# Kernel tuning notes

Hardware: AMD Instinct MI355X
Metric: run time of the kernel (lower is better)

The kernel has to match this reference:

```python
import jax, jax.numpy as jnp
import numpy as np

B, V, C, D = 32, 64, 32, 256
VOCAB = 20000
NUM_T = 1000


def _run_lstm(x, Wih, Whh, b):
    # x: [T, B, H_in]; torch-style single-layer LSTM with zero initial state
    T, Bb, _ = x.shape
    H = Whh.shape[1]
    def step(carry, xt):
        h, c = carry
        z = xt @ Wih.T + h @ Whh.T + b
        i, f, g, o = jnp.split(z, 4, axis=-1)
        c = jax.nn.sigmoid(f) * c + jax.nn.sigmoid(i) * jnp.tanh(g)
        h = jax.nn.sigmoid(o) * jnp.tanh(c)
        return (h, c), h
    h0 = jnp.zeros((Bb, H), x.dtype)
    _, ys = jax.lax.scan(step, (h0, h0), x)
    return ys


def _forward(input_seqs, masks, lengths, seq_time_step, code_masks, emb, WQ1, WK1,
             decay, initial, lstm_Wih, lstm_Whh, lstm_b, hs_Wih, hs_Whh, hs_b,
             whk_W, whk_b, w1_W, w1_b, w2_W, w2_b, fuse_W, fuse_b, lab_W, lab_b,
             betas, Wdiff, diffusion_time_t, normal_noise):
    Bb, Vv, Cc = input_seqs.shape
    tok = input_seqs.reshape(-1, Cc)                      # [B*V, C]
    x = emb[tok]                                          # [B*V, C, D]
    q = x @ WQ1.T
    k = x @ WK1.T
    dp = jnp.einsum('bcd,bed->bce', q, k)                 # [B*V, C, C]
    cm = code_masks.reshape(-1, Cc)
    dp = dp - cm[:, None, :] - cm[:, :, None]
    sp = jax.nn.softmax(dp / jnp.sqrt(jnp.float32(D)), axis=-1)
    femb = jnp.einsum('bce,bed->bcd', sp, x)              # attended code embeddings
    femb = ((cm - 1e20) / -1e20)[:, :, None] * femb       # zero out padded codes
    dec = decay[tok][..., None]                           # [B*V, C, 1]
    ini = initial[tok][..., None]
    t = seq_time_step.reshape(-1)[:, None, None]          # [B*V, 1, 1]
    gate = jax.nn.sigmoid(dec * t + ini)                  # time-decay gate
    vv = jnp.einsum('bcx,bcd->bd', gate, femb)            # [B*V, D] visit vector
    vv = vv.reshape(Bb, Vv, -1).transpose(1, 0, 2)        # [V, B, D]

    lstm_out = _run_lstm(vv, lstm_Wih, lstm_Whh, lstm_b)  # [V, B, D]
    t_lstm = lstm_out.transpose(1, 0, 2)                  # [B, V, D]
    hiddenstate = _run_lstm(lstm_out, hs_Wih, hs_Whh, hs_b).transpose(1, 0, 2)

    # Vectorized form of the original per-step python loop.
    # NOTE: the original always uses e_k = t_lstm_out[:, 0:1, :] (step 0) -- kept faithfully.
    e_k = t_lstm[:, 0:1, :]                               # [B, 1, D]
    whp = hiddenstate[:, :-1, :] @ whk_W.T + whk_b        # [B, V-1, D]
    cat = jnp.concatenate([jnp.broadcast_to(e_k, whp.shape), whp], axis=-1)
    attn = jax.nn.softmax(jnp.tanh(cat @ w1_W.T + w1_b) @ w2_W.T + w2_b, axis=-1)
    rest = e_k * attn[..., 0:1] + whp * attn[..., 1:2]
    aligned = jnp.concatenate([e_k, rest], axis=1)        # [B, V, D]

    alpha = jnp.cumprod(1.0 - betas)[diffusion_time_t][:, None, None]
    noisy = aligned * jnp.sqrt(alpha) + normal_noise * jnp.sqrt(1.0 - alpha)
    predicted_noise = noisy @ Wdiff                       # surrogate for UNetModel (source not provided)
    gen = aligned + (normal_noise - predicted_noise)

    fused = jnp.concatenate([t_lstm, gen], axis=-1) @ fuse_W.T + fuse_b   # [B, V, D]
    mask_final = (jnp.arange(Vv)[None, :] == (lengths - 1)[:, None]).astype(fused.dtype)
    final = (fused * mask_final[:, :, None]).sum(axis=1)  # select last valid visit
    return final @ lab_W.T + lab_b                        # [B, 2]


def setup_inputs() -> dict:
    key = jax.random.key(0)
    ks = jax.random.split(key, 20)
    s = 0.05
    n = lambda i, shp: jax.random.normal(ks[i], shp, jnp.float32) * s
    emb = jax.random.normal(ks[0], (VOCAB + 1, D), jnp.float32) * 0.02
    emb = emb.at[VOCAB].set(0.0)  # padding_idx row
    return {
        'input_seqs': jax.random.randint(ks[1], (B, V, C), 0, VOCAB),
        'masks': jnp.zeros((B, V), jnp.float32),
        'lengths': jax.random.randint(ks[2], (B,), 1, V + 1),
        'seq_time_step': jax.random.uniform(ks[3], (B, V), jnp.float32),
        'code_masks': jnp.zeros((B, V, C), jnp.float32),
        'emb': emb,
        'WQ1': n(4, (D, D)), 'WK1': n(5, (D, D)),
        'decay': jnp.full((VOCAB + 1,), -0.1, jnp.float32),
        'initial': jnp.full((VOCAB + 1,), 1.0, jnp.float32),
        'lstm_Wih': n(6, (4 * D, D)), 'lstm_Whh': n(7, (4 * D, D)),
        'lstm_b': jnp.zeros((4 * D,), jnp.float32),
        'hs_Wih': n(8, (4 * D, D)), 'hs_Whh': n(9, (4 * D, D)),
        'hs_b': jnp.zeros((4 * D,), jnp.float32),
        'whk_W': n(10, (D, D)), 'whk_b': jnp.zeros((D,), jnp.float32),
        'w1_W': n(11, (64, 2 * D)), 'w1_b': jnp.zeros((64,), jnp.float32),
        'w2_W': n(12, (2, 64)), 'w2_b': jnp.zeros((2,), jnp.float32),
        'fuse_W': n(13, (D, 2 * D)), 'fuse_b': jnp.zeros((D,), jnp.float32),
        'lab_W': n(14, (2, D)), 'lab_b': jnp.zeros((2,), jnp.float32),
        'betas': jnp.linspace(1e-4, 0.02, NUM_T, dtype=jnp.float32),
        'Wdiff': n(15, (D, D)),
        'diffusion_time_t': jax.random.randint(ks[16], (B,), 0, NUM_T),
        'normal_noise': jax.random.normal(ks[17], (B, V, D), jnp.float32),
    }


def reference(input_seqs, masks, lengths, seq_time_step, code_masks, emb, WQ1, WK1,
              decay, initial, lstm_Wih, lstm_Whh, lstm_b, hs_Wih, hs_Whh, hs_b,
              whk_W, whk_b, w1_W, w1_b, w2_W, w2_b, fuse_W, fuse_b, lab_W, lab_b,
              betas, Wdiff, diffusion_time_t, normal_noise):
    return _forward(input_seqs, masks, lengths, seq_time_step, code_masks, emb, WQ1, WK1,
                    decay, initial, lstm_Wih, lstm_Whh, lstm_b, hs_Wih, hs_Whh, hs_b,
                    whk_W, whk_b, w1_W, w1_b, w2_W, w2_b, fuse_W, fuse_b, lab_W, lab_b,
                    betas, Wdiff, diffusion_time_t, normal_noise)
```

## Files before the change

kernel.cpp:

```cpp
#include <hip/hip_runtime.h>
#include <hip/hip_bf16.h>
#include <cmath>

typedef __attribute__((ext_vector_type(8))) short bf16x8;
typedef __attribute__((ext_vector_type(4))) float f32x4;
typedef __attribute__((ext_vector_type(4))) int i32x4;
typedef __attribute__((ext_vector_type(2))) unsigned int u32x2;

__device__ __forceinline__ float bf2f(unsigned short u) {
    unsigned int x = ((unsigned int)u) << 16;
    return __builtin_bit_cast(float, x);
}
__device__ __forceinline__ unsigned short f2bf(float f) {
    unsigned int x = __builtin_bit_cast(unsigned int, f);
    unsigned int lsb = (x >> 16) & 1u;
    x += 0x7fffu + lsb;
    return (unsigned short)(x >> 16);
}
__device__ __forceinline__ float sigm(float z) {
    return 1.f / (1.f + __expf(-z));
}
__device__ __forceinline__ float rcpf(float x) { return __builtin_amdgcn_rcpf(x); }
__device__ __forceinline__ float sigm_f(float z) { return rcpf(1.f + __expf(-z)); }
__device__ __forceinline__ float tanh_f(float z) { return 1.f - 2.f * rcpf(1.f + __expf(2.f * z)); }

__device__ __forceinline__ long ldg_sc8l(const void* p) {
    long r;
    asm volatile("global_load_dwordx2 %0, %1, off sc1" : "=v"(r) : "v"(p) : "memory");
    return r;
}
__device__ __forceinline__ u32x2 ldg_sc_u2(const void* p) {
    u32x2 r;
    asm volatile("global_load_dwordx2 %0, %1, off sc1" : "=v"(r) : "v"(p) : "memory");
    return r;
}
__device__ __forceinline__ void stg_sc_u2(void* p, u32x2 v) {
    asm volatile("global_store_dwordx2 %0, %1, off sc1" :: "v"(p), "v"(v) : "memory");
}
__device__ __forceinline__ void stg_sc_b(void* p, int v) {
    asm volatile("global_store_byte %0, %1, off sc1" :: "v"(p), "v"(v) : "memory");
}

__global__ void __launch_bounds__(256) pack_all(
    const float* __restrict__ Whh1, const float* __restrict__ Wih2,
    const float* __restrict__ Whh2, const float* __restrict__ Wih1,
    const float* __restrict__ WQ1, const float* __restrict__ WK1,
    const float* __restrict__ betas, const int* __restrict__ dift,
    const float* __restrict__ whk_W, const float* __restrict__ fuse_W,
    const float* __restrict__ w1_W,
    long* __restrict__ Wq, float* __restrict__ cs,
    unsigned short* __restrict__ W1h, unsigned short* __restrict__ M_pk,
    float* __restrict__ alpha, int* __restrict__ flags,
    float* __restrict__ whkT, float* __restrict__ fuseT,
    float* __restrict__ w1T) {
    int blk = blockIdx.x, tid = threadIdx.x;
    if (blk < 384) {
        int R = blk * 8 + (tid >> 5);
        int mat = R >> 10;
        int n = R & 1023;
        int t32 = tid & 31;
        const float* src = (mat == 0) ? Whh1 : (mat == 1 ? Wih2 : Whh2);
        const float* rp = src + (size_t)n * 256 + t32 * 8;
        float v[8];
        float mx = 0.f;
        for (int j = 0; j < 8; ++j) { v[j] = rp[j]; mx = fmaxf(mx, fabsf(v[j])); }
        for (int m = 1; m <= 16; m <<= 1) mx = fmaxf(mx, __shfl_xor(mx, m));
        float inv = mx > 0.f ? 127.f / mx : 0.f;
        unsigned int lo = 0, hi = 0;
        for (int j = 0; j < 4; ++j) {
            int iv = __float2int_rn(v[j] * inv);
            lo |= ((unsigned int)(unsigned char)(signed char)iv) << (8 * j);
            int iv2 = __float2int_rn(v[4 + j] * inv);
            hi |= ((unsigned int)(unsigned char)(signed char)iv2) << (8 * j);
        }
        int g = n >> 8, rem = n & 255;
        int w8 = rem >> 5, dt = (rem >> 4) & 1, cc = rem & 15;
        int t8 = g * 2 + dt;
        int kb = t32 >> 2, q = t32 & 3;
        unsigned int* dst = (unsigned int*)Wq +
            ((size_t)((mat * 512 + w8 * 64 + t8 * 8 + kb) * 64) + q * 16 + cc) * 2;
        dst[0] = lo;
        dst[1] = hi;
        if (t32 == 0) cs[mat * 1024 + n] = mx / 16129.f;
    } else if (blk < 512) {
        int cch = (blk - 384) * 256 + tid;
        int nt = cch >> 9;
        int r = cch & 511;
        int kb = r >> 6;
        int lane = r & 63;
        int grow = nt * 16 + (lane & 15);
        int k0 = kb * 32 + (lane >> 4) * 8;
        const float* sp = Wih1 + (size_t)grow * 256 + k0;
        bf16x8 hi;
        for (int j = 0; j < 8; ++j) hi[j] = (short)f2bf(sp[j]);
        *reinterpret_cast<bf16x8*>(W1h + (size_t)cch * 8) = hi;
    } else if (blk == 512) {
        if (tid < 32) {
            int tb = dift[tid];
            float p = 1.f;
            for (int i = 0; i <= tb; ++i) p *= (1.f - betas[i]);
            alpha[tid] = p;
        }
    } else if (blk == 513) {
        for (int i = tid; i < 4096; i += 256) flags[i] = 0;
    } else if (blk < 578) {
        int gid = (blk - 514) * 256 + tid;
        for (int i = 0; i < 4; ++i) {
            int e = gid + i * 16384;
            int k = e >> 8, dd = e & 255;
            whkT[e] = whk_W[(size_t)dd * 256 + k];
        }
    } else if (blk < 706) {
        int gid = (blk - 578) * 256 + tid;
        for (int i = 0; i < 4; ++i) {
            int e = gid + i * 32768;
            int k = e >> 8, dd = e & 255;
            fuseT[e] = fuse_W[(size_t)dd * 512 + k];
        }
    } else if (blk < 738) {
        int gid = (blk - 706) * 256 + tid;
        for (int i = 0; i < 4; ++i) {
            int e = gid + i * 8192;
            int k = e >> 6, j = e & 63;
            w1T[e] = w1_W[(size_t)j * 512 + k];
        }
    } else {
        __shared__ unsigned short As[256][32];
        __shared__ unsigned short Bs[256][32];
        int bx = blk - 738;
        int e0 = (bx >> 3) << 5;
        int f0 = (bx & 7) << 5;
        int col = tid & 31, rr = tid >> 5;
        for (int rep = 0; rep < 32; ++rep) {
            int d = rep * 8 + rr;
            As[d][col] = f2bf(WQ1[d * 256 + e0 + col]);
            Bs[d][col] = f2bf(WK1[d * 256 + f0 + col]);
        }
        __syncthreads();
        int el = tid & 31;
        int fl0 = tid >> 5;
        for (int i = 0; i < 4; ++i) {
            int fl = fl0 + 8 * i;
            float acc = 0.f;
            for (int d = 0; d < 256; ++d)
                acc += bf2f(As[d][el]) * bf2f(Bs[d][fl]);
            int e = e0 + el, f = f0 + fl;
            int kb = e >> 5, r = (e >> 3) & 3, j = e & 7;
            int nb = f >> 4;
            int lane = (r << 4) | (f & 15);
            M_pk[(((nb * 8 + kb) * 64) + lane) * 8 + j] = f2bf(acc);
        }
    }
}

__global__ void __launch_bounds__(256) eprep(const float* __restrict__ emb,
                                             const unsigned short* __restrict__ M_pk,
                                             unsigned short* __restrict__ Ep) {
    __shared__ __align__(16) unsigned short x_bf[32 * 256];
    int v0 = blockIdx.x * 32;
    int tid = threadIdx.x;
    for (int it = 0; it < 8; ++it) {
        int fidx = it * 256 + tid;
        int cc = fidx >> 6;
        int f4 = fidx & 63;
        int row = v0 + cc;
        float4 vx = make_float4(0.f, 0.f, 0.f, 0.f);
        if (row < 20001)
            vx = *(reinterpret_cast<const float4*>(emb + (size_t)row * 256) + f4);
        int colx = f4 * 4;
        ushort4 w;
        w.x = f2bf(vx.x); w.y = f2bf(vx.y); w.z = f2bf(vx.z); w.w = f2bf(vx.w);
        *reinterpret_cast<ushort4*>(&x_bf[cc * 256 + (colx ^ ((cc & 7) << 3))]) = w;
    }
    __syncthreads();
    int wv = tid >> 6, lane = tid & 63, lr = lane & 15, lk = lane >> 4;
    f32x4 acc[2][4];
    for (int a = 0; a < 2; ++a)
        for (int n = 0; n < 4; ++n) acc[a][n] = (f32x4){0.f, 0.f, 0.f, 0.f};
    for (int kb = 0; kb < 8; ++kb) {
        bf16x8 afr[2];
        for (int mb = 0; mb < 2; ++mb) {
            int row = mb * 16 + lr;
            int colx = kb * 32 + lk * 8;
            afr[mb] = *reinterpret_cast<const bf16x8*>(&x_bf[row * 256 + (colx ^ ((row & 7) << 3))]);
        }
        for (int nbi = 0; nbi < 4; ++nbi) {
            int nb = wv * 4 + nbi;
            bf16x8 bfr = *reinterpret_cast<const bf16x8*>(M_pk + (((nb * 8 + kb) * 64) + lane) * 8);
            acc[0][nbi] = __builtin_amdgcn_mfma_f32_16x16x32_bf16(afr[0], bfr, acc[0][nbi], 0, 0, 0);
            acc[1][nbi] = __builtin_amdgcn_mfma_f32_16x16x32_bf16(afr[1], bfr, acc[1][nbi], 0, 0, 0);
        }
    }
    for (int mb = 0; mb < 2; ++mb)
        for (int nbi = 0; nbi < 4; ++nbi)
            for (int r = 0; r < 4; ++r) {
                int row = mb * 16 + lk * 4 + r;
                int col = wv * 64 + nbi * 16 + lr;
                if (v0 + row < 20001)
                    Ep[(size_t)(v0 + row) * 256 + col] = f2bf(acc[mb][nbi][r]);
            }
}

__global__ void __launch_bounds__(256) attn_bags(
    const int* __restrict__ seqs, const float* __restrict__ tstep,
    const float* __restrict__ cmask, const float* __restrict__ emb,
    const float* __restrict__ decay, const float* __restrict__ initial,
    const unsigned short* __restrict__ Ep, float* __restrict__ vv) {
    __shared__ __align__(16) unsigned short x_bf[32 * 256];
    __shared__ __align__(16) unsigned short t1_bf[32 * 256];
    __shared__ float dp_f[32 * 33];
    __shared__ float gate_sh[32];
    __shared__ float cm_sh[32];
    __shared__ int tok_sh[32];
    __shared__ float w_sh[32];

    int bag = blockIdx.x;
    int tid = threadIdx.x;

    if (tid < 32) {
        int tok = seqs[bag * 32 + tid];
        tok_sh[tid] = tok;
        float cm = cmask[bag * 32 + tid];
        cm_sh[tid] = cm;
        float tt = tstep[bag];
        float g = sigm(decay[tok] * tt + initial[tok]);
        g *= (cm - 1e20f) / (-1e20f);
        gate_sh[tid] = g;
    }
    __syncthreads();

    for (int it = 0; it < 8; ++it) {
        int fidx = it * 256 + tid;
        int c = fidx >> 6;
        int f4 = fidx & 63;
        const float4* src = reinterpret_cast<const float4*>(emb + (size_t)tok_sh[c] * 256) + f4;
        float4 vx = *src;
        int colx = f4 * 4;
        int eidx = c * 256 + (colx ^ ((c & 7) << 3));
        ushort4 w;
        w.x = f2bf(vx.x); w.y = f2bf(vx.y); w.z = f2bf(vx.z); w.w = f2bf(vx.w);
        *reinterpret_cast<ushort4*>(&x_bf[eidx]) = w;
    }
    for (int it = 0; it < 4; ++it) {
        int idx = it * 256 + tid;
        int cc = idx >> 5;
        int colx = (idx & 31) * 8;
        bf16x8 e = *reinterpret_cast<const bf16x8*>(Ep + (size_t)tok_sh[cc] * 256 + colx);
        *reinterpret_cast<bf16x8*>(&t1_bf[cc * 256 + (colx ^ ((cc & 7) << 3))]) = e;
    }
    __syncthreads();

    int wv = tid >> 6;
    int lane = tid & 63;
    int lr = lane & 15;
    int lk = lane >> 4;

    {
        int mb = wv >> 1, nb2 = wv & 1;
        f32x4 dacc = (f32x4){0.f, 0.f, 0.f, 0.f};
        for (int kb = 0; kb < 8; ++kb) {
            int cola = kb * 32 + lk * 8;
            int rowa = mb * 16 + lr;
            bf16x8 afr = *reinterpret_cast<const bf16x8*>(&t1_bf[rowa * 256 + (cola ^ ((rowa & 7) << 3))]);
            int rowb = nb2 * 16 + lr;
            bf16x8 bfr = *reinterpret_cast<const bf16x8*>(&x_bf[rowb * 256 + (cola ^ ((rowb & 7) << 3))]);
            dacc = __builtin_amdgcn_mfma_f32_16x16x32_bf16(afr, bfr, dacc, 0, 0, 0);
        }
        for (int r = 0; r < 4; ++r) {
            int c = mb * 16 + lk * 4 + r;
            int e = nb2 * 16 + lr;
            dp_f[c * 33 + e] = dacc[r];
        }
    }
    __syncthreads();

    if (tid < 32) {
        int c = tid;
        float cmc = cm_sh[c];
        float lg[32];
        float mx = -1e30f;
        for (int e = 0; e < 32; ++e) {
            float l = (dp_f[c * 33 + e] - cmc - cm_sh[e]) * 0.0625f;
            lg[e] = l;
            mx = fmaxf(mx, l);
        }
        float s = 0.f;
        for (int e = 0; e < 32; ++e) { float ex = __expf(lg[e] - mx); lg[e] = ex; s += ex; }
        float inv = 1.f / s;
        for (int e = 0; e < 32; ++e) dp_f[c * 33 + e] = lg[e] * inv;
    }
    __syncthreads();
    if (tid < 32) {
        int e = tid;
        float a2 = 0.f;
        for (int c = 0; c < 32; ++c) a2 += gate_sh[c] * dp_f[c * 33 + e];
        w_sh[e] = a2;
    }
    __syncthreads();

    float accv = 0.f;
    int d = tid;
    for (int e = 0; e < 32; ++e)
        accv += w_sh[e] * bf2f(x_bf[e * 256 + (d ^ ((e & 7) << 3))]);
    vv[(size_t)bag * 256 + d] = accv;
}

__global__ void __launch_bounds__(256) x1_mfma(const float* __restrict__ vv,
                                               const unsigned short* __restrict__ W1h,
                                               const float* __restrict__ lstm_b,
                                               unsigned short* __restrict__ X1bf) {
    __shared__ __align__(16) unsigned short xs[32 * 256];
    int blk = blockIdx.x;
    int rb = blk >> 3, gb = blk & 7;
    int tid = threadIdx.x;
    for (int it = 0; it < 8; ++it) {
        int idx = it * 256 + tid;
        int row = idx >> 6, f4 = idx & 63;
        float4 v = *reinterpret_cast<const float4*>(vv + (size_t)(rb * 32 + row) * 256 + f4 * 4);
        ushort4 w;
        w.x = f2bf(v.x); w.y = f2bf(v.y); w.z = f2bf(v.z); w.w = f2bf(v.w);
        *reinterpret_cast<ushort4*>(&xs[row * 256 + ((f4 * 4) ^ ((row & 7) << 3))]) = w;
    }
    __syncthreads();
    int wv = tid >> 6, lane = tid & 63, cl = lane & 15, kh = lane >> 4;
    f32x4 acc[2][2];
    for (int n = 0; n < 2; ++n) {
        int nt = gb * 8 + wv * 2 + n;
        float bz = lstm_b[nt * 16 + cl];
        acc[n][0] = (f32x4){bz, bz, bz, bz};
        acc[n][1] = (f32x4){bz, bz, bz, bz};
    }
    #pragma unroll
    for (int kb = 0; kb < 8; ++kb) {
        int k = kb * 32 + kh * 8;
        bf16x8 a0 = *reinterpret_cast<const bf16x8*>(&xs[cl * 256 + (k ^ ((cl & 7) << 3))]);
        bf16x8 a1 = *reinterpret_cast<const bf16x8*>(&xs[(16 + cl) * 256 + (k ^ (((16 + cl) & 7) << 3))]);
        for (int n = 0; n < 2; ++n) {
            int nt = gb * 8 + wv * 2 + n;
            size_t o = ((size_t)(nt * 8 + kb) * 64 + lane) * 8;
            bf16x8 bh = *reinterpret_cast<const bf16x8*>(W1h + o);
            acc[n][0] = __builtin_amdgcn_mfma_f32_16x16x32_bf16(a0, bh, acc[n][0], 0, 0, 0);
            acc[n][1] = __builtin_amdgcn_mfma_f32_16x16x32_bf16(a1, bh, acc[n][1], 0, 0, 0);
        }
    }
    for (int n = 0; n < 2; ++n) {
        int nt = gb * 8 + wv * 2 + n;
        int g = nt * 16 + cl;
        int dX = g & 255, gt = g >> 8;
        for (int mt = 0; mt < 2; ++mt)
            for (int r = 0; r < 4; ++r) {
                int row = rb * 32 + mt * 16 + kh * 4 + r;
                int b = row >> 6, t = row & 63;
                X1bf[((size_t)t * 32 + b) * 1024 + dX * 4 + gt] = f2bf(acc[n][mt][r]);
            }
    }
}

__global__ void __launch_bounds__(512, 1) lstm_persist(
    const long* __restrict__ Wq, const float* __restrict__ cs,
    const unsigned short* __restrict__ X1bf, const float* __restrict__ hs_b,
    const int* __restrict__ lengths,
    unsigned short* __restrict__ h1bf, unsigned short* __restrict__ h2bf,
    signed char* h1q, unsigned short* p1, int* flags) {
    int role = blockIdx.x;
    int half = role & 1;
    int kind = role >> 1;
    int tid = threadIdx.x;
    int w = tid >> 6, lane = tid & 63, c = lane & 15, q = lane >> 4;

    long wt[64];
    #pragma unroll
    for (int t8 = 0; t8 < 8; ++t8)
        #pragma unroll
        for (int kb = 0; kb < 8; ++kb)
            wt[t8 * 8 + kb] = Wq[(size_t)((kind * 512 + w * 64 + t8 * 8 + kb) * 64) + lane];
    float csv[8];
    #pragma unroll
    for (int t8 = 0; t8 < 8; ++t8) {
        int g = t8 >> 1, dt = t8 & 1;
        csv[t8] = cs[kind * 1024 + g * 256 + w * 32 + dt * 16 + c];
    }

    if (kind == 0) {
        __shared__ signed char hq[2][16][272];
        float cstate[8] = {0.f, 0.f, 0.f, 0.f, 0.f, 0.f, 0.f, 0.f};
        int B0 = half * 16 + q * 4;
        int dbase = w * 32;
        int vstar[4];
        #pragma unroll
        for (int r = 0; r < 4; ++r) vstar[r] = lengths[B0 + r] - 1;
        for (int t = 0; t < 64; ++t) {
            ushort4 xv[8];
            #pragma unroll
            for (int dt = 0; dt < 2; ++dt)
                #pragma unroll
                for (int r = 0; r < 4; ++r) {
                    int B = B0 + r, d = dbase + dt * 16 + c;
                    xv[dt * 4 + r] = *reinterpret_cast<const ushort4*>(
                        X1bf + ((size_t)(t * 32 + B) * 1024 + d * 4));
                }
            i32x4 acc[8];
            #pragma unroll
            for (int i = 0; i < 8; ++i) acc[i] = (i32x4){0, 0, 0, 0};
            if (t > 0) {
                int pb = (t - 1) & 1;
                long a[8];
                #pragma unroll
                for (int kb = 0; kb < 8; ++kb)
                    a[kb] = *reinterpret_cast<const long*>(&hq[pb][c][kb * 32 + q * 8]);
                #pragma unroll
                for (int t8 = 0; t8 < 8; ++t8)
                    #pragma unroll
                    for (int kb = 0; kb < 8; ++kb)
                        acc[t8] = __builtin_amdgcn_mfma_i32_16x16x32_i8(
                            a[kb], wt[t8 * 8 + kb], acc[t8], 0, 0, 0);
            }
            #pragma unroll
            for (int dt = 0; dt < 2; ++dt)
                #pragma unroll
                for (int r = 0; r < 4; ++r) {
                    int idx = dt * 4 + r;
                    ushort4 x = xv[idx];
                    float zi = (float)acc[0 + dt][r] * csv[0 + dt] + bf2f(x.x);
                    float zf = (float)acc[2 + dt][r] * csv[2 + dt] + bf2f(x.y);
                    float zg = (float)acc[4 + dt][r] * csv[4 + dt] + bf2f(x.z);
                    float zo = (float)acc[6 + dt][r] * csv[6 + dt] + bf2f(x.w);
                    float cn = sigm_f(zf) * cstate[idx] + sigm_f(zi) * tanh_f(zg);
                    float hn = sigm_f(zo) * tanh_f(cn);
                    cstate[idx] = cn;
                    int B = B0 + r, d = dbase + dt * 16 + c;
                    if (t == 0 || t == vstar[r])
                        h1bf[(size_t)(t * 32 + B) * 256 + d] = f2bf(hn);
                    int hv = __float2int_rn(hn * 127.f);
                    hq[t & 1][q * 4 + r][d] = (signed char)hv;
                    stg_sc_b(h1q + (size_t)(t * 32 + B) * 256 + d, hv);
                }
            asm volatile("s_waitcnt vmcnt(0)" ::: "memory");
            if (lane == 0)
                __hip_atomic_store(flags + t * 16 + half * 8 + w, 1,
                                   __ATOMIC_RELAXED, __HIP_MEMORY_SCOPE_AGENT);
            __syncthreads();
        }
    } else if (kind == 1) {
        long acur[8], anext[8];
        {
            const int* f = flags + half * 8;
            while (1) {
                int v = 1;
                if (lane < 8)
                    v = __hip_atomic_load(f + lane, __ATOMIC_RELAXED, __HIP_MEMORY_SCOPE_AGENT);
                if (__all(v != 0)) break;
                __builtin_amdgcn_s_sleep(1);
            }
            __builtin_amdgcn_sched_barrier(0);
            const signed char* hb = h1q + (size_t)(half * 16) * 256;
            #pragma unroll
            for (int kb = 0; kb < 8; ++kb)
                acur[kb] = ldg_sc8l(hb + c * 256 + kb * 32 + q * 8);
            asm volatile("s_waitcnt vmcnt(0)" ::: "memory");
            __builtin_amdgcn_sched_barrier(0);
        }
        for (int s = 0; s < 64; ++s) {
            if (s < 63) {
                const int* f = flags + (s + 1) * 16 + half * 8;
                while (1) {
                    int v = 1;
                    if (lane < 8)
                        v = __hip_atomic_load(f + lane, __ATOMIC_RELAXED, __HIP_MEMORY_SCOPE_AGENT);
                    if (__all(v != 0)) break;
                    __builtin_amdgcn_s_sleep(1);
                }
                __builtin_amdgcn_sched_barrier(0);
                const signed char* hb = h1q + (size_t)((s + 1) * 32 + half * 16) * 256;
                #pragma unroll
                for (int kb = 0; kb < 8; ++kb)
                    anext[kb] = ldg_sc8l(hb + c * 256 + kb * 32 + q * 8);
            }
            i32x4 acc[8];
            #pragma unroll
            for (int i = 0; i < 8; ++i) acc[i] = (i32x4){0, 0, 0, 0};
            #pragma unroll
            for (int t8 = 0; t8 < 8; ++t8)
                #pragma unroll
                for (int kb = 0; kb < 8; ++kb)
                    acc[t8] = __builtin_amdgcn_mfma_i32_16x16x32_i8(
                        acur[kb], wt[t8 * 8 + kb], acc[t8], 0, 0, 0);
            #pragma unroll
            for (int t8 = 0; t8 < 8; ++t8) {
                int g = t8 >> 1, dt = t8 & 1;
                int n = g * 256 + w * 32 + dt * 16 + c;
                u32x2 pv;
                pv.x = (unsigned int)f2bf((float)acc[t8][0] * csv[t8]) |
                       ((unsigned int)f2bf((float)acc[t8][1] * csv[t8]) << 16);
                pv.y = (unsigned int)f2bf((float)acc[t8][2] * csv[t8]) |
                       ((unsigned int)f2bf((float)acc[t8][3] * csv[t8]) << 16);
                stg_sc_u2(p1 + ((size_t)(s * 2 + half) * 1024 + n) * 16 + q * 4, pv);
            }
            asm volatile("s_waitcnt vmcnt(0)" ::: "memory");
            __builtin_amdgcn_sched_barrier(0);
            if (lane == 0)
                __hip_atomic_store(flags + 1024 + s * 16 + half * 8 + w, 1,
                                   __ATOMIC_RELAXED, __HIP_MEMORY_SCOPE_AGENT);
            #pragma unroll
            for (int kb = 0; kb < 8; ++kb) acur[kb] = anext[kb];
        }
    } else {
        __shared__ signed char hq2[2][16][272];
        float cstate[8] = {0.f, 0.f, 0.f, 0.f, 0.f, 0.f, 0.f, 0.f};
        float bias[8];
        #pragma unroll
        for (int t8 = 0; t8 < 8; ++t8) {
            int g = t8 >> 1, dt = t8 & 1;
            bias[t8] = hs_b[g * 256 + w * 32 + dt * 16 + c];
        }
        int B0 = half * 16 + q * 4;
        int dbase = w * 32;
        int vstar[4];
        #pragma unroll
        for (int r = 0; r < 4; ++r) vstar[r] = lengths[B0 + r] - 1;
        u32x2 pvc[8], pvn[8];
        {
            const int* fp = flags + 1024 + half * 8 + w;
            while (__hip_atomic_load(fp, __ATOMIC_RELAXED, __HIP_MEMORY_SCOPE_AGENT) == 0)
                __builtin_amdgcn_s_sleep(1);
            __builtin_amdgcn_sched_barrier(0);
            #pragma unroll
            for (int t8 = 0; t8 < 8; ++t8) {
                int g = t8 >> 1, dt = t8 & 1;
                int n = g * 256 + w * 32 + dt * 16 + c;
                pvc[t8] = ldg_sc_u2(p1 + ((size_t)half * 1024 + n) * 16 + q * 4);
            }
        }
        for (int s = 0; s < 64; ++s) {
            if (s < 63) {
                const int* fp = flags + 1024 + (s + 1) * 16 + half * 8 + w;
                while (__hip_atomic_load(fp, __ATOMIC_RELAXED, __HIP_MEMORY_SCOPE_AGENT) == 0)
                    __builtin_amdgcn_s_sleep(1);
                __builtin_amdgcn_sched_barrier(0);
                #pragma unroll
                for (int t8 = 0; t8 < 8; ++t8) {
                    int g = t8 >> 1, dt = t8 & 1;
                    int n = g * 256 + w * 32 + dt * 16 + c;
                    pvn[t8] = ldg_sc_u2(p1 + ((size_t)((s + 1) * 2 + half) * 1024 + n) * 16 + q * 4);
                }
                asm volatile("s_waitcnt vmcnt(8)" ::: "memory");
            } else {
                asm volatile("s_waitcnt vmcnt(0)" ::: "memory");
            }
            __builtin_amdgcn_sched_barrier(0);
            i32x4 acc[8];
            #pragma unroll
            for (int i = 0; i < 8; ++i) acc[i] = (i32x4){0, 0, 0, 0};
            if (s > 0) {
                int pb = (s - 1) & 1;
                long a[8];
                #pragma unroll
                for (int kb = 0; kb < 8; ++kb)
                    a[kb] = *reinterpret_cast<const long*>(&hq2[pb][c][kb * 32 + q * 8]);
                #pragma unroll
                for (int t8 = 0; t8 < 8; ++t8)
                    #pragma unroll
                    for (int kb = 0; kb < 8; ++kb)
                        acc[t8] = __builtin_amdgcn_mfma_i32_16x16x32_i8(
                            a[kb], wt[t8 * 8 + kb], acc[t8], 0, 0, 0);
            }
            #pragma unroll
            for (int dt = 0; dt < 2; ++dt)
                #pragma unroll
                for (int r = 0; r < 4; ++r) {
                    int idx = dt * 4 + r;
                    float p_i = bf2f((unsigned short)((r < 2 ? pvc[0 + dt].x : pvc[0 + dt].y) >> ((r & 1) * 16)));
                    float p_f = bf2f((unsigned short)((r < 2 ? pvc[2 + dt].x : pvc[2 + dt].y) >> ((r & 1) * 16)));
                    float p_g = bf2f((unsigned short)((r < 2 ? pvc[4 + dt].x : pvc[4 + dt].y) >> ((r & 1) * 16)));
                    float p_o = bf2f((unsigned short)((r < 2 ? pvc[6 + dt].x : pvc[6 + dt].y) >> ((r & 1) * 16)));
                    float zi = (float)acc[0 + dt][r] * csv[0 + dt] + p_i + bias[0 + dt];
                    float zf = (float)acc[2 + dt][r] * csv[2 + dt] + p_f + bias[2 + dt];
                    float zg = (float)acc[4 + dt][r] * csv[4 + dt] + p_g + bias[4 + dt];
                    float zo = (float)acc[6 + dt][r] * csv[6 + dt] + p_o + bias[6 + dt];
                    float cn = sigm_f(zf) * cstate[idx] + sigm_f(zi) * tanh_f(zg);
                    float hn = sigm_f(zo) * tanh_f(cn);
                    cstate[idx] = cn;
                    int B = B0 + r, d = dbase + dt * 16 + c;
                    if (s == vstar[r] - 1)
                        h2bf[(size_t)(s * 32 + B) * 256 + d] = f2bf(hn);
                    hq2[s & 1][q * 4 + r][d] = (signed char)__float2int_rn(hn * 127.f);
                }
            __syncthreads();
            #pragma unroll
            for (int t8 = 0; t8 < 8; ++t8) pvc[t8] = pvn[t8];
        }
    }
}

__global__ void __launch_bounds__(256) tail_k(
    const int* __restrict__ lengths,
    const unsigned short* __restrict__ h1, const unsigned short* __restrict__ h2,
    const float* __restrict__ whkT, const float* __restrict__ whk_b,
    const float* __restrict__ w1T, const float* __restrict__ w1_b,
    const float* __restrict__ w2_W, const float* __restrict__ w2_b,
    const float* __restrict__ fuseT, const float* __restrict__ fuse_b,
    const float* __restrict__ lab_W, const float* __restrict__ lab_b,
    const float* __restrict__ Wdiff, const float* __restrict__ alpha,
    const float* __restrict__ noise, float* __restrict__ out) {
    __shared__ float ek[256], tv[256], hs[256], whp[256], a1s[64];
    __shared__ float noisy_s[256], fin[512], fused_s[256], attn_s[2];
    int b = blockIdx.x, tid = threadIdx.x;
    int vstar = lengths[b] - 1;
    {
        ek[tid] = bf2f(h1[(size_t)b * 256 + tid]);
        tv[tid] = bf2f(h1[((size_t)vstar * 32 + b) * 256 + tid]);
        if (vstar > 0)
            hs[tid] = bf2f(h2[((size_t)(vstar - 1) * 32 + b) * 256 + tid]);
    }
    __syncthreads();

    float aligned;
    if (vstar > 0) {
        float s0 = 0.f, s1 = 0.f, s2 = 0.f, s3 = 0.f;
        for (int k = 0; k < 256; k += 4) {
            s0 += whkT[(k + 0) * 256 + tid] * hs[k + 0];
            s1 += whkT[(k + 1) * 256 + tid] * hs[k + 1];
            s2 += whkT[(k + 2) * 256 + tid] * hs[k + 2];
            s3 += whkT[(k + 3) * 256 + tid] * hs[k + 3];
        }
        whp[tid] = whk_b[tid] + s0 + s1 + s2 + s3;
        __syncthreads();
        if (tid < 64) {
            float a0 = 0.f, a1 = 0.f, a2 = 0.f, a3 = 0.f;
            for (int k = 0; k < 256; k += 4) {
                a0 += w1T[(k + 0) * 64 + tid] * ek[k + 0];
                a1 += w1T[(k + 1) * 64 + tid] * ek[k + 1];
                a2 += w1T[(k + 2) * 64 + tid] * ek[k + 2];
                a3 += w1T[(k + 3) * 64 + tid] * ek[k + 3];
            }
            for (int k = 0; k < 256; k += 4) {
                a0 += w1T[(256 + k + 0) * 64 + tid] * whp[k + 0];
                a1 += w1T[(256 + k + 1) * 64 + tid] * whp[k + 1];
                a2 += w1T[(256 + k + 2) * 64 + tid] * whp[k + 2];
                a3 += w1T[(256 + k + 3) * 64 + tid] * whp[k + 3];
            }
            a1s[tid] = tanhf(w1_b[tid] + a0 + a1 + a2 + a3);
        }
        __syncthreads();
        if (tid < 2) {
            float a3 = w2_b[tid];
            const float* wr2 = w2_W + tid * 64;
            for (int k = 0; k < 64; ++k) a3 += wr2[k] * a1s[k];
            attn_s[tid] = a3;
        }
        __syncthreads();
        float m = fmaxf(attn_s[0], attn_s[1]);
        float e0 = __expf(attn_s[0] - m), e1 = __expf(attn_s[1] - m);
        float inv = 1.f / (e0 + e1);
        aligned = ek[tid] * (e0 * inv) + whp[tid] * (e1 * inv);
    } else {
        aligned = ek[tid];
    }

    float al = alpha[b];
    float sa = sqrtf(al), sb = sqrtf(1.f - al);
    float nz = noise[((size_t)b * 64 + vstar) * 256 + tid];
    noisy_s[tid] = aligned * sa + nz * sb;
    __syncthreads();
    {
        float p0 = 0.f, p1v = 0.f, p2 = 0.f, p3 = 0.f;
        for (int k = 0; k < 256; k += 4) {
            p0 += noisy_s[k + 0] * Wdiff[(size_t)(k + 0) * 256 + tid];
            p1v += noisy_s[k + 1] * Wdiff[(size_t)(k + 1) * 256 + tid];
            p2 += noisy_s[k + 2] * Wdiff[(size_t)(k + 2) * 256 + tid];
            p3 += noisy_s[k + 3] * Wdiff[(size_t)(k + 3) * 256 + tid];
        }
        float gen = aligned + nz - (p0 + p1v + p2 + p3);
        fin[tid] = tv[tid];
        fin[256 + tid] = gen;
    }
    __syncthreads();
    {
        float f0 = 0.f, f1 = 0.f, f2 = 0.f, f3 = 0.f;
        for (int k = 0; k < 512; k += 4) {
            f0 += fuseT[(k + 0) * 256 + tid] * fin[k + 0];
            f1 += fuseT[(k + 1) * 256 + tid] * fin[k + 1];
            f2 += fuseT[(k + 2) * 256 + tid] * fin[k + 2];
            f3 += fuseT[(k + 3) * 256 + tid] * fin[k + 3];
        }
        fused_s[tid] = fuse_b[tid] + f0 + f1 + f2 + f3;
    }
    __syncthreads();
    if (tid < 2) {
        float o = lab_b[tid];
        const float* lw = lab_W + tid * 256;
        for (int k = 0; k < 256; ++k) o += lw[k] * fused_s[k];
        out[b * 2 + tid] = o;
    }
}

extern "C" void kernel_launch(void* const* d_in, const int* in_sizes, int n_in,
                              void* d_out, int out_size, void* d_ws, size_t ws_size,
                              hipStream_t stream) {
    const int*   seqs    = (const int*)  d_in[0];
    const int*   lengths = (const int*)  d_in[2];
    const float* tstep   = (const float*)d_in[3];
    const float* cmask   = (const float*)d_in[4];
    const float* emb     = (const float*)d_in[5];
    const float* WQ1     = (const float*)d_in[6];
    const float* WK1     = (const float*)d_in[7];
    const float* decay   = (const float*)d_in[8];
    const float* initial = (const float*)d_in[9];
    const float* Wih1    = (const float*)d_in[10];
    const float* Whh1    = (const float*)d_in[11];
    const float* lstm_b  = (const float*)d_in[12];
    const float* Wih2    = (const float*)d_in[13];
    const float* Whh2    = (const float*)d_in[14];
    const float* hs_b    = (const float*)d_in[15];
    const float* whk_W   = (const float*)d_in[16];
    const float* whk_b   = (const float*)d_in[17];
    const float* w1_W    = (const float*)d_in[18];
    const float* w1_b    = (const float*)d_in[19];
    const float* w2_W    = (const float*)d_in[20];
    const float* w2_b    = (const float*)d_in[21];
    const float* fuse_W  = (const float*)d_in[22];
    const float* fuse_b  = (const float*)d_in[23];
    const float* lab_W   = (const float*)d_in[24];
    const float* lab_b   = (const float*)d_in[25];
    const float* betas   = (const float*)d_in[26];
    const float* Wdiff   = (const float*)d_in[27];
    const int*   dift    = (const int*)  d_in[28];
    const float* noise   = (const float*)d_in[29];
    float* out = (float*)d_out;

    float* ws = (float*)d_ws;
    size_t off = 0;
    auto alloc = [&](size_t nfloats) { size_t r = off; off += (nfloats + 63) & ~(size_t)63; return r; };
    unsigned short* M_pk  = (unsigned short*)(ws + alloc(32768));
    float*          alpha = ws + alloc(64);
    float*          cs    = ws + alloc(3072);
    int*            flags = (int*)(ws + alloc(4096));
    float*          vv    = ws + alloc(524288);
    unsigned short* X1bf  = (unsigned short*)(ws + alloc(1048576));
    unsigned short* h1bf  = (unsigned short*)(ws + alloc(262144));
    unsigned short* h2bf  = (unsigned short*)(ws + alloc(262144));
    unsigned short* p1    = (unsigned short*)(ws + alloc(1048576));
    long*           Wq    = (long*)(ws + alloc(196608));
    unsigned short* W1h   = (unsigned short*)(ws + alloc(131072));
    float*          whkT  = ws + alloc(65536);
    float*          fuseT = ws + alloc(131072);
    float*          w1T   = ws + alloc(32768);
    signed char*    h1q   = (signed char*)(ws + alloc(131072));
    unsigned short* Ep    = (unsigned short*)(ws + alloc(2560128));

    pack_all<<<802, 256, 0, stream>>>(Whh1, Wih2, Whh2, Wih1, WQ1, WK1, betas, dift,
                                      whk_W, fuse_W, w1_W,
                                      Wq, cs, W1h, M_pk, alpha, flags,
                                      whkT, fuseT, w1T);
    eprep<<<626, 256, 0, stream>>>(emb, M_pk, Ep);
    attn_bags<<<2048, 256, 0, stream>>>(seqs, tstep, cmask, emb, decay, initial, Ep, vv);
    x1_mfma<<<512, 256, 0, stream>>>(vv, W1h, lstm_b, X1bf);
    lstm_persist<<<6, 512, 0, stream>>>(Wq, cs, X1bf, hs_b, lengths,
                                        h1bf, h2bf, h1q, p1, flags);
    tail_k<<<32, 256, 0, stream>>>(lengths, h1bf, h2bf, whkT, whk_b,
                                   w1T, w1_b, w2_W, w2_b, fuseT, fuse_b,
                                   lab_W, lab_b, Wdiff, alpha, noise, out);
}
```

Measured before the change: 365.3 us.

## Co-locate LSTM1 recurrence and layer-2 input projection in one block via LDS

```diff
diff --git a/kernel.cpp b/kernel.cpp
--- a/kernel.cpp
+++ b/kernel.cpp
@@ -24,11 +24,6 @@
 __device__ __forceinline__ float sigm_f(float z) { return rcpf(1.f + __expf(-z)); }
 __device__ __forceinline__ float tanh_f(float z) { return 1.f - 2.f * rcpf(1.f + __expf(2.f * z)); }
 
-__device__ __forceinline__ long ldg_sc8l(const void* p) {
-    long r;
-    asm volatile("global_load_dwordx2 %0, %1, off sc1" : "=v"(r) : "v"(p) : "memory");
-    return r;
-}
 __device__ __forceinline__ u32x2 ldg_sc_u2(const void* p) {
     u32x2 r;
     asm volatile("global_load_dwordx2 %0, %1, off sc1" : "=v"(r) : "v"(p) : "memory");
@@ -36,9 +31,6 @@
 }
 __device__ __forceinline__ void stg_sc_u2(void* p, u32x2 v) {
     asm volatile("global_store_dwordx2 %0, %1, off sc1" :: "v"(p), "v"(v) : "memory");
-}
-__device__ __forceinline__ void stg_sc_b(void* p, int v) {
-    asm volatile("global_store_byte %0, %1, off sc1" :: "v"(p), "v"(v) : "memory");
 }
 
 __global__ void __launch_bounds__(256) pack_all(
@@ -356,156 +348,148 @@
     }
 }
 
-__global__ void __launch_bounds__(512, 1) lstm_persist(
+__global__ void __launch_bounds__(1024, 4) lstm_persist(
     const long* __restrict__ Wq, const float* __restrict__ cs,
     const unsigned short* __restrict__ X1bf, const float* __restrict__ hs_b,
     const int* __restrict__ lengths,
     unsigned short* __restrict__ h1bf, unsigned short* __restrict__ h2bf,
-    signed char* h1q, unsigned short* p1, int* flags) {
-    int role = blockIdx.x;
-    int half = role & 1;
-    int kind = role >> 1;
+    unsigned short* p1, int* flags) {
+    int blk = blockIdx.x;
     int tid = threadIdx.x;
-    int w = tid >> 6, lane = tid & 63, c = lane & 15, q = lane >> 4;
-
-    long wt[64];
-    #pragma unroll
-    for (int t8 = 0; t8 < 8; ++t8)
+    int lane = tid & 63, c = lane & 15, q = lane >> 4;
+
+    if (blk < 2) {
+        __shared__ signed char hq[2][16][272];
+        int half = blk;
+        int w16 = tid >> 6;
+        bool isA = w16 < 8;
+        int wl = w16 & 7;
+        int kind = isA ? 0 : 1;
+
+        long wt[64];
         #pragma unroll
-        for (int kb = 0; kb < 8; ++kb)
-            wt[t8 * 8 + kb] = Wq[(size_t)((kind * 512 + w * 64 + t8 * 8 + kb) * 64) + lane];
-    float csv[8];
-    #pragma unroll
-    for (int t8 = 0; t8 < 8; ++t8) {
-        int g = t8 >> 1, dt = t8 & 1;
-        csv[t8] = cs[kind * 1024 + g * 256 + w * 32 + dt * 16 + c];
-    }
-
-    if (kind == 0) {
-        __shared__ signed char hq[2][16][272];
-        float cstate[8] = {0.f, 0.f, 0.f, 0.f, 0.f, 0.f, 0.f, 0.f};
-        int B0 = half * 16 + q * 4;
-        int dbase = w * 32;
-        int vstar[4];
+        for (int t8 = 0; t8 < 8; ++t8)
+            #pragma unroll
+            for (int kb = 0; kb < 8; ++kb)
+                wt[t8 * 8 + kb] = Wq[(size_t)((kind * 512 + wl * 64 + t8 * 8 + kb) * 64) + lane];
+        float csv[8];
         #pragma unroll
-        for (int r = 0; r < 4; ++r) vstar[r] = lengths[B0 + r] - 1;
-        for (int t = 0; t < 64; ++t) {
-            ushort4 xv[8];
+        for (int t8 = 0; t8 < 8; ++t8) {
+            int g = t8 >> 1, dt = t8 & 1;
+            csv[t8] = cs[kind * 1024 + g * 256 + wl * 32 + dt * 16 + c];
+        }
+
+        if (isA) {
+            float cstate[8] = {0.f, 0.f, 0.f, 0.f, 0.f, 0.f, 0.f, 0.f};
+            int B0 = half * 16 + q * 4;
+            int dbase = wl * 32;
+            int vstar[4];
             #pragma unroll
-            for (int dt = 0; dt < 2; ++dt)
-                #pragma unroll
-                for (int r = 0; r < 4; ++r) {
-                    int B = B0 + r, d = dbase + dt * 16 + c;
-                    xv[dt * 4 + r] = *reinterpret_cast<const ushort4*>(
-                        X1bf + ((size_t)(t * 32 + B) * 1024 + d * 4));
+            for (int r = 0; r < 4; ++r) vstar[r] = lengths[B0 + r] - 1;
+            for (int p = 0; p <= 64; ++p) {
+                if (p < 64) {
+                    int t = p;
+                    ushort4 xv[8];
+                    #pragma unroll
+                    for (int dt = 0; dt < 2; ++dt)
+                        #pragma unroll
+                        for (int r = 0; r < 4; ++r) {
+                            int B = B0 + r, d = dbase + dt * 16 + c;
+                            xv[dt * 4 + r] = *reinterpret_cast<const ushort4*>(
+                                X1bf + ((size_t)(t * 32 + B) * 1024 + d * 4));
+                        }
+                    i32x4 acc[8];
+                    #pragma unroll
+                    for (int i = 0; i < 8; ++i) acc[i] = (i32x4){0, 0, 0, 0};
+                    if (t > 0) {
+                        int pb = (t - 1) & 1;
+                        long a[8];
+                        #pragma unroll
+                        for (int kb = 0; kb < 8; ++kb)
+                            a[kb] = *reinterpret_cast<const long*>(&hq[pb][c][kb * 32 + q * 8]);
+                        #pragma unroll
+                        for (int t8 = 0; t8 < 8; ++t8)
+                            #pragma unroll
+                            for (int kb = 0; kb < 8; ++kb)
+                                acc[t8] = __builtin_amdgcn_mfma_i32_16x16x32_i8(
+                                    a[kb], wt[t8 * 8 + kb], acc[t8], 0, 0, 0);
+                    }
+                    #pragma unroll
+                    for (int dt = 0; dt < 2; ++dt)
+                        #pragma unroll
+                        for (int r = 0; r < 4; ++r) {
+                            int idx = dt * 4 + r;
+                            ushort4 x = xv[idx];
+                            float zi = (float)acc[0 + dt][r] * csv[0 + dt] + bf2f(x.x);
+                            float zf = (float)acc[2 + dt][r] * csv[2 + dt] + bf2f(x.y);
+                            float zg = (float)acc[4 + dt][r] * csv[4 + dt] + bf2f(x.z);
+                            float zo = (float)acc[6 + dt][r] * csv[6 + dt] + bf2f(x.w);
+                            float cn = sigm_f(zf) * cstate[idx] + sigm_f(zi) * tanh_f(zg);
+                            float hn = sigm_f(zo) * tanh_f(cn);
+                            cstate[idx] = cn;
+                            int B = B0 + r, d = dbase + dt * 16 + c;
+                            if (t == 0 || t == vstar[r])
+                                h1bf[(size_t)(t * 32 + B) * 256 + d] = f2bf(hn);
+                            hq[t & 1][q * 4 + r][d] = (signed char)__float2int_rn(hn * 127.f);
+                        }
                 }
-            i32x4 acc[8];
-            #pragma unroll
-            for (int i = 0; i < 8; ++i) acc[i] = (i32x4){0, 0, 0, 0};
-            if (t > 0) {
-                int pb = (t - 1) & 1;
-                long a[8];
-                #pragma unroll
-                for (int kb = 0; kb < 8; ++kb)
-                    a[kb] = *reinterpret_cast<const long*>(&hq[pb][c][kb * 32 + q * 8]);
-                #pragma unroll
-                for (int t8 = 0; t8 < 8; ++t8)
+                __syncthreads();
+            }
+        } else {
+            for (int p = 0; p <= 64; ++p) {
+                int s = p - 1;
+                if (p >= 1) {
+                    long a[8];
                     #pragma unroll
                     for (int kb = 0; kb < 8; ++kb)
-                        acc[t8] = __builtin_amdgcn_mfma_i32_16x16x32_i8(
-                            a[kb], wt[t8 * 8 + kb], acc[t8], 0, 0, 0);
-            }
-            #pragma unroll
-            for (int dt = 0; dt < 2; ++dt)
-                #pragma unroll
-                for (int r = 0; r < 4; ++r) {
-                    int idx = dt * 4 + r;
-                    ushort4 x = xv[idx];
-                    float zi = (float)acc[0 + dt][r] * csv[0 + dt] + bf2f(x.x);
-                    float zf = (float)acc[2 + dt][r] * csv[2 + dt] + bf2f(x.y);
-                    float zg = (float)acc[4 + dt][r] * csv[4 + dt] + bf2f(x.z);
-                    float zo = (float)acc[6 + dt][r] * csv[6 + dt] + bf2f(x.w);
-                    float cn = sigm_f(zf) * cstate[idx] + sigm_f(zi) * tanh_f(zg);
-                    float hn = sigm_f(zo) * tanh_f(cn);
-                    cstate[idx] = cn;
-                    int B = B0 + r, d = dbase + dt * 16 + c;
-                    if (t == 0 || t == vstar[r])
-                        h1bf[(size_t)(t * 32 + B) * 256 + d] = f2bf(hn);
-                    int hv = __float2int_rn(hn * 127.f);
-                    hq[t & 1][q * 4 + r][d] = (signed char)hv;
-                    stg_sc_b(h1q + (size_t)(t * 32 + B) * 256 + d, hv);
+                        a[kb] = *reinterpret_cast<const long*>(&hq[s & 1][c][kb * 32 + q * 8]);
+                    i32x4 acc[8];
+                    #pragma unroll
+                    for (int i = 0; i < 8; ++i) acc[i] = (i32x4){0, 0, 0, 0};
+                    #pragma unroll
+                    for (int t8 = 0; t8 < 8; ++t8)
+                        #pragma unroll
+                        for (int kb = 0; kb < 8; ++kb)
+                            acc[t8] = __builtin_amdgcn_mfma_i32_16x16x32_i8(
+                                a[kb], wt[t8 * 8 + kb], acc[t8], 0, 0, 0);
+                    #pragma unroll
+                    for (int t8 = 0; t8 < 8; ++t8) {
+                        int g = t8 >> 1, dt = t8 & 1;
+                        int n = g * 256 + wl * 32 + dt * 16 + c;
+                        u32x2 pv;
+                        pv.x = (unsigned int)f2bf((float)acc[t8][0] * csv[t8]) |
+                               ((unsigned int)f2bf((float)acc[t8][1] * csv[t8]) << 16);
+                        pv.y = (unsigned int)f2bf((float)acc[t8][2] * csv[t8]) |
+                               ((unsigned int)f2bf((float)acc[t8][3] * csv[t8]) << 16);
+                        stg_sc_u2(p1 + ((size_t)(s * 2 + half) * 1024 + n) * 16 + q * 4, pv);
+                    }
                 }
-            asm volatile("s_waitcnt vmcnt(0)" ::: "memory");
-            if (lane == 0)
-                __hip_atomic_store(flags + t * 16 + half * 8 + w, 1,
-                                   __ATOMIC_RELAXED, __HIP_MEMORY_SCOPE_AGENT);
-            __syncthreads();
-        }
-    } else if (kind == 1) {
-        long acur[8], anext[8];
-        {
-            const int* f = flags + half * 8;
-            while (1) {
-                int v = 1;
-                if (lane < 8)
-                    v = __hip_atomic_load(f + lane, __ATOMIC_RELAXED, __HIP_MEMORY_SCOPE_AGENT);
-                if (__all(v != 0)) break;
-                __builtin_amdgcn_s_sleep(1);
-            }
-            __builtin_amdgcn_sched_barrier(0);
-            const signed char* hb = h1q + (size_t)(half * 16) * 256;
+                __syncthreads();
+                if (p >= 1 && lane == 0)
+                    __hip_atomic_store(flags + 1024 + s * 16 + half * 8 + wl, 1,
+                                       __ATOMIC_RELAXED, __HIP_MEMORY_SCOPE_AGENT);
+            }
+        }
+    } else {
+        int half = blk - 2;
+        int w = tid >> 6;
+        if (w >= 8) {
+            for (int s = 0; s < 64; ++s) __syncthreads();
+            return;
+        }
+        __shared__ signed char hq2[2][16][272];
+        long wt[64];
+        #pragma unroll
+        for (int t8 = 0; t8 < 8; ++t8)
             #pragma unroll
             for (int kb = 0; kb < 8; ++kb)
-                acur[kb] = ldg_sc8l(hb + c * 256 + kb * 32 + q * 8);
-            asm volatile("s_waitcnt vmcnt(0)" ::: "memory");
-            __builtin_amdgcn_sched_barrier(0);
-        }
-        for (int s = 0; s < 64; ++s) {
-            if (s < 63) {
-                const int* f = flags + (s + 1) * 16 + half * 8;
-                while (1) {
-                    int v = 1;
-                    if (lane < 8)
-                        v = __hip_atomic_load(f + lane, __ATOMIC_RELAXED, __HIP_MEMORY_SCOPE_AGENT);
-                    if (__all(v != 0)) break;
-                    __builtin_amdgcn_s_sleep(1);
-                }
-                __builtin_amdgcn_sched_barrier(0);
-                const signed char* hb = h1q + (size_t)((s + 1) * 32 + half * 16) * 256;
-                #pragma unroll
-                for (int kb = 0; kb < 8; ++kb)
-                    anext[kb] = ldg_sc8l(hb + c * 256 + kb * 32 + q * 8);
-            }
-            i32x4 acc[8];
-            #pragma unroll
-            for (int i = 0; i < 8; ++i) acc[i] = (i32x4){0, 0, 0, 0};
-            #pragma unroll
-            for (int t8 = 0; t8 < 8; ++t8)
-                #pragma unroll
-                for (int kb = 0; kb < 8; ++kb)
-                    acc[t8] = __builtin_amdgcn_mfma_i32_16x16x32_i8(
-                        acur[kb], wt[t8 * 8 + kb], acc[t8], 0, 0, 0);
-            #pragma unroll
-            for (int t8 = 0; t8 < 8; ++t8) {
-                int g = t8 >> 1, dt = t8 & 1;
-                int n = g * 256 + w * 32 + dt * 16 + c;
-                u32x2 pv;
-                pv.x = (unsigned int)f2bf((float)acc[t8][0] * csv[t8]) |
-                       ((unsigned int)f2bf((float)acc[t8][1] * csv[t8]) << 16);
-                pv.y = (unsigned int)f2bf((float)acc[t8][2] * csv[t8]) |
-                       ((unsigned int)f2bf((float)acc[t8][3] * csv[t8]) << 16);
-                stg_sc_u2(p1 + ((size_t)(s * 2 + half) * 1024 + n) * 16 + q * 4, pv);
-            }
-            asm volatile("s_waitcnt vmcnt(0)" ::: "memory");
-            __builtin_amdgcn_sched_barrier(0);
-            if (lane == 0)
-                __hip_atomic_store(flags + 1024 + s * 16 + half * 8 + w, 1,
-                                   __ATOMIC_RELAXED, __HIP_MEMORY_SCOPE_AGENT);
-            #pragma unroll
-            for (int kb = 0; kb < 8; ++kb) acur[kb] = anext[kb];
-        }
-    } else {
-        __shared__ signed char hq2[2][16][272];
+                wt[t8 * 8 + kb] = Wq[(size_t)((2 * 512 + w * 64 + t8 * 8 + kb) * 64) + lane];
+        float csv[8];
+        #pragma unroll
+        for (int t8 = 0; t8 < 8; ++t8) {
+            int g = t8 >> 1, dt = t8 & 1;
+            csv[t8] = cs[2 * 1024 + g * 256 + w * 32 + dt * 16 + c];
+        }
         float cstate[8] = {0.f, 0.f, 0.f, 0.f, 0.f, 0.f, 0.f, 0.f};
         float bias[8];
         #pragma unroll
@@ -745,7 +729,6 @@
     float*          whkT  = ws + alloc(65536);
     float*          fuseT = ws + alloc(131072);
     float*          w1T   = ws + alloc(32768);
-    signed char*    h1q   = (signed char*)(ws + alloc(131072));
     unsigned short* Ep    = (unsigned short*)(ws + alloc(2560128));
 
     pack_all<<<802, 256, 0, stream>>>(Whh1, Wih2, Whh2, Wih1, WQ1, WK1, betas, dift,
@@ -755,8 +738,8 @@
     eprep<<<626, 256, 0, stream>>>(emb, M_pk, Ep);
     attn_bags<<<2048, 256, 0, stream>>>(seqs, tstep, cmask, emb, decay, initial, Ep, vv);
     x1_mfma<<<512, 256, 0, stream>>>(vv, W1h, lstm_b, X1bf);
-    lstm_persist<<<6, 512, 0, stream>>>(Wq, cs, X1bf, hs_b, lengths,
-                                        h1bf, h2bf, h1q, p1, flags);
+    lstm_persist<<<4, 1024, 0, stream>>>(Wq, cs, X1bf, hs_b, lengths,
+                                         h1bf, h2bf, p1, flags);
     tail_k<<<32, 256, 0, stream>>>(lengths, h1bf, h2bf, whkT, whk_b,
                                    w1T, w1_b, w2_W, w2_b, fuseT, fuse_b,
                                    lab_W, lab_b, Wdiff, alpha, noise, out);
```

Result: slower. 928.5 us (+154.2%).
